# Kernel optimization log

Hardware: AMD Instinct MI355X
Metric: run time of the kernel (lower is better)

## Reference

```python
import jax, jax.numpy as jnp
import numpy as np

IN_DIM, H_DIM, EMB_DIM, CHEB_K = 2, 64, 10, 3
B, L, N = 16, 12, 2048
CAT = IN_DIM + H_DIM


def setup_inputs() -> dict:
    key = jax.random.key(0)
    ks = jax.random.split(key, 7)
    x = jax.random.normal(ks[0], (B, L, N, IN_DIM), dtype=jnp.float32)
    node_embs = jax.random.normal(ks[1], (N, EMB_DIM), dtype=jnp.float32)
    As = jax.random.uniform(ks[2], (N, N), dtype=jnp.float32) / N  # row-stochastic-ish support
    # NAPL parameter pools (AGCRN-style): per-gate weight/bias pools indexed by node embedding
    s = 0.1
    Wg_pool = jax.random.normal(ks[3], (EMB_DIM, CHEB_K, CAT, 2 * H_DIM), dtype=jnp.float32) * s
    bg_pool = jax.random.normal(ks[4], (EMB_DIM, 2 * H_DIM), dtype=jnp.float32) * s
    Wc_pool = jax.random.normal(ks[5], (EMB_DIM, CHEB_K, CAT, H_DIM), dtype=jnp.float32) * s
    bc_pool = jax.random.normal(ks[6], (EMB_DIM, H_DIM), dtype=jnp.float32) * s
    return {"x": x, "node_embs": node_embs, "As": As,
            "Wg_pool": Wg_pool, "bg_pool": bg_pool,
            "Wc_pool": Wc_pool, "bc_pool": bc_pool}


def _cheb_supports(A, k):
    # T0 = I, T1 = A, T_j = 2 A T_{j-1} - T_{j-2}
    n = A.shape[0]
    Ts = [jnp.eye(n, dtype=A.dtype), A]
    for _ in range(2, k):
        Ts.append(2.0 * A @ Ts[-1] - Ts[-2])
    return jnp.stack(Ts[:k], axis=0)  # (K, N, N)


def _napl_conv(xin, supports, Wn, bn):
    # xin: (B,N,Ci); supports: (K,N,N); Wn: (N,K,Ci,Co); bn: (N,Co)
    xg = jnp.einsum('knm,bmc->bnkc', supports, xin)
    return jnp.einsum('bnki,nkio->bno', xg, Wn) + bn


def reference(x, node_embs, As, Wg_pool, bg_pool, Wc_pool, bc_pool):
    supports = _cheb_supports(As, CHEB_K)
    # node-adaptive parameters (time-invariant: hoist out of the recurrence)
    Wg = jnp.einsum('nd,dkio->nkio', node_embs, Wg_pool)  # (N,K,CAT,2H)
    bg = node_embs @ bg_pool                               # (N,2H)
    Wc = jnp.einsum('nd,dkio->nkio', node_embs, Wc_pool)  # (N,K,CAT,H)
    bc = node_embs @ bc_pool                               # (N,H)

    def step(h_prev, x_t):
        cat = jnp.concatenate([h_prev, x_t], axis=-1)      # (B,N,CAT)
        gate = jax.nn.sigmoid(_napl_conv(cat, supports, Wg, bg))
        r_t, u_t = jnp.split(gate, 2, axis=-1)
        cat2 = jnp.concatenate([r_t * h_prev, x_t], axis=-1)
        c_t = jnp.tanh(_napl_conv(cat2, supports, Wc, bc))
        h_t = u_t * h_prev + (1.0 - u_t) * c_t
        return h_t, h_t

    h0 = jnp.zeros((x.shape[0], x.shape[2], H_DIM), dtype=x.dtype)
    x_time = jnp.moveaxis(x, 1, 0)                          # (L,B,N,C)
    h_n, outs = jax.lax.scan(step, h0, x_time)
    output = jnp.moveaxis(outs, 0, 1)                       # (B,L,N,H)
    return output, h_n
```

## Files before the change

### kernel.cpp

```cpp
#include <hip/hip_runtime.h>
#include <cstdint>
#include <cstddef>

typedef _Float16 h16;
typedef h16 v8h __attribute__((ext_vector_type(8)));
typedef h16 v4h __attribute__((ext_vector_type(4)));
typedef float v4f __attribute__((ext_vector_type(4)));

constexpr int NN = 2048;
constexpr float INV_N = 1.0f / 2048.0f;
constexpr int LP = 72;

#define MFMA16(a, b, c) __builtin_amdgcn_mfma_f32_16x16x32_f16((a), (b), (c), 0, 0, 0)

__global__ void fill_k(float* __restrict__ o, float v, size_t ntot) {
  size_t i = (size_t)blockIdx.x * 256 + threadIdx.x;
  if (i < ntot) o[i] = v;
}


__global__ void prep_Asplit_k(const float* __restrict__ A,
                              h16* __restrict__ hi, h16* __restrict__ lo) {
  int tid = blockIdx.x * 256 + threadIdx.x;
  float v = A[tid] * 2048.0f;
  h16 h = (h16)v;
  hi[tid] = h;
  lo[tid] = (h16)(v - (float)h);
}

__global__ void prep_AsTsplit_k(const float* __restrict__ A,
                                h16* __restrict__ hi, h16* __restrict__ lo) {
  int tid = blockIdx.x * 256 + threadIdx.x;
  int t = tid & 2047, j = tid >> 11;
  float v = A[(size_t)t * NN + j] * 2048.0f;
  h16 h = (h16)v;
  hi[(size_t)j * NN + t] = h;
  lo[(size_t)j * NN + t] = (h16)(v - (float)h);
}

__global__ void prep_x0split_k(const float* __restrict__ x,
                               h16* __restrict__ hi, h16* __restrict__ lo) {
  int tid = blockIdx.x * 256 + threadIdx.x;
  int n = tid & 2047, c = tid >> 11;
  int ii = c & 1, b = (c >> 1) & 15, lt = c >> 5;
  float v = x[(((size_t)(b * 12 + lt)) * NN + n) * 2 + ii];
  h16 h = (h16)v;
  hi[tid] = h;
  lo[tid] = (h16)(v - (float)h);
}

template<int CO>
__global__ void prep_wpack_k(const float* __restrict__ Wp,
                             h16* __restrict__ Ph, h16* __restrict__ Pl) {
  int tid = blockIdx.x * 256 + threadIdx.x;
  int c = tid & 7;
  int ln = (tid >> 3) & 63;
  int rest = tid >> 9;
  int b = rest & 3;
  int kk = (rest >> 2) & 1;
  int r3 = rest >> 3;
  int t = r3 % 30;
  int g = r3 / 30;
  int o = g * 64 + b * 16 + (ln & 15);
  int kcol = (t / 3) * 192 + (t % 3) * 64 + kk * 32 + (ln >> 4) * 8 + c;
  int d = kcol / 192, rem = kcol - d * 192;
  int jb = rem >> 6, i = rem & 63;
  float v;
  if (jb == 0)
    v = Wp[((size_t)((d * 3 + 0) * 66 + i)) * CO + o] -
        Wp[((size_t)((d * 3 + 2) * 66 + i)) * CO + o];
  else if (jb == 1)
    v = Wp[((size_t)((d * 3 + 1) * 66 + i)) * CO + o];
  else
    v = 2.f * Wp[((size_t)((d * 3 + 2) * 66 + i)) * CO + o];
  h16 h = (h16)v;
  Ph[tid] = h;
  Pl[tid] = (h16)(v - (float)h);
}

template<int CO>
__global__ void prep_wx_k(const float* __restrict__ E, const float* __restrict__ Wp,
                          float* __restrict__ Wx) {
  int tid = blockIdx.x * 256 + threadIdx.x;
  int o = tid & (CO - 1), t6 = (tid / CO) % 6, n = tid / (6 * CO);
  int k = t6 >> 1, ii = t6 & 1;
  float s = 0.f;
  for (int d = 0; d < 10; ++d) {
    float p0 = Wp[((size_t)((d * 3 + 0) * 66 + 64 + ii)) * CO + o];
    float p1 = Wp[((size_t)((d * 3 + 1) * 66 + 64 + ii)) * CO + o];
    float p2 = Wp[((size_t)((d * 3 + 2) * 66 + 64 + ii)) * CO + o];
    float v = (k == 0) ? (p0 - p2) : (k == 1 ? p1 : 2.f * p2);
    s += E[n * 10 + d] * v;
  }
  Wx[tid] = s;
}

template<int CO>
__global__ void prep_b_k(const float* __restrict__ E, const float* __restrict__ bp,
                         float* __restrict__ bv) {
  int tid = blockIdx.x * 256 + threadIdx.x;
  int o = tid & (CO - 1), n = tid / CO;
  float s = 0.f;
  for (int d = 0; d < 10; ++d) s += E[n * 10 + d] * bp[d * CO + o];
  bv[tid] = s;
}

template<int OM>
__global__ __launch_bounds__(256, 4) void sgemm_k(
    const h16* __restrict__ Ih, const h16* __restrict__ Il,
    const h16* __restrict__ Bh, const h16* __restrict__ Bl,
    float* __restrict__ oF, h16* __restrict__ oH, h16* __restrict__ oL,
    float* __restrict__ xsv, int xoff) {
  const int m0 = blockIdx.x * 64, n0 = blockIdx.y * 64;
  __shared__ __align__(16) h16 sAh[64 * LP], sAl[64 * LP];
  __shared__ __align__(16) h16 sBh[64 * LP], sBl[64 * LP];
  const int tid = threadIdx.x, lane = tid & 63, w = tid >> 6;
  const int wm = w >> 1, wn = w & 1;
  v4f acc[2][2] = {};
  const int sr = tid >> 2, sc = (tid & 3) * 16;
  v8h rah0 = *(const v8h*)(Ih + (size_t)(m0 + sr) * NN + sc);
  v8h rah1 = *(const v8h*)(Ih + (size_t)(m0 + sr) * NN + sc + 8);
  v8h ral0 = *(const v8h*)(Il + (size_t)(m0 + sr) * NN + sc);
  v8h ral1 = *(const v8h*)(Il + (size_t)(m0 + sr) * NN + sc + 8);
  v8h rbh0 = *(const v8h*)(Bh + (size_t)(n0 + sr) * NN + sc);
  v8h rbh1 = *(const v8h*)(Bh + (size_t)(n0 + sr) * NN + sc + 8);
  v8h rbl0 = *(const v8h*)(Bl + (size_t)(n0 + sr) * NN + sc);
  v8h rbl1 = *(const v8h*)(Bl + (size_t)(n0 + sr) * NN + sc + 8);
  for (int kt = 0; kt < NN; kt += 64) {
    __syncthreads();
    *(v8h*)(sAh + sr * LP + sc) = rah0;
    *(v8h*)(sAh + sr * LP + sc + 8) = rah1;
    *(v8h*)(sAl + sr * LP + sc) = ral0;
    *(v8h*)(sAl + sr * LP + sc + 8) = ral1;
    *(v8h*)(sBh + sr * LP + sc) = rbh0;
    *(v8h*)(sBh + sr * LP + sc + 8) = rbh1;
    *(v8h*)(sBl + sr * LP + sc) = rbl0;
    *(v8h*)(sBl + sr * LP + sc + 8) = rbl1;
    __syncthreads();
    if (kt + 64 < NN) {
      const int k2 = kt + 64 + sc;
      rah0 = *(const v8h*)(Ih + (size_t)(m0 + sr) * NN + k2);
      rah1 = *(const v8h*)(Ih + (size_t)(m0 + sr) * NN + k2 + 8);
      ral0 = *(const v8h*)(Il + (size_t)(m0 + sr) * NN + k2);
      ral1 = *(const v8h*)(Il + (size_t)(m0 + sr) * NN + k2 + 8);
      rbh0 = *(const v8h*)(Bh + (size_t)(n0 + sr) * NN + k2);
      rbh1 = *(const v8h*)(Bh + (size_t)(n0 + sr) * NN + k2 + 8);
      rbl0 = *(const v8h*)(Bl + (size_t)(n0 + sr) * NN + k2);
      rbl1 = *(const v8h*)(Bl + (size_t)(n0 + sr) * NN + k2 + 8);
    }
#pragma unroll
    for (int kk = 0; kk < 2; ++kk) {
      const int ko = kk * 32 + (lane >> 4) * 8;
      const int rs = lane & 15;
      v8h Ah0 = *(const v8h*)(sAh + (wm * 32 + rs) * LP + ko);
      v8h Ah1 = *(const v8h*)(sAh + (wm * 32 + 16 + rs) * LP + ko);
      v8h Al0 = *(const v8h*)(sAl + (wm * 32 + rs) * LP + ko);
      v8h Al1 = *(const v8h*)(sAl + (wm * 32 + 16 + rs) * LP + ko);
      v8h Bh0 = *(const v8h*)(sBh + (wn * 32 + rs) * LP + ko);
      v8h Bh1 = *(const v8h*)(sBh + (wn * 32 + 16 + rs) * LP + ko);
      v8h Bl0 = *(const v8h*)(sBl + (wn * 32 + rs) * LP + ko);
      v8h Bl1 = *(const v8h*)(sBl + (wn * 32 + 16 + rs) * LP + ko);
      acc[0][0] = MFMA16(Ah0, Bh0, acc[0][0]);
      acc[0][1] = MFMA16(Ah0, Bh1, acc[0][1]);
      acc[1][0] = MFMA16(Ah1, Bh0, acc[1][0]);
      acc[1][1] = MFMA16(Ah1, Bh1, acc[1][1]);
      acc[0][0] = MFMA16(Al0, Bh0, acc[0][0]);
      acc[0][1] = MFMA16(Al0, Bh1, acc[0][1]);
      acc[1][0] = MFMA16(Al1, Bh0, acc[1][0]);
      acc[1][1] = MFMA16(Al1, Bh1, acc[1][1]);
      acc[0][0] = MFMA16(Ah0, Bl0, acc[0][0]);
      acc[0][1] = MFMA16(Ah0, Bl1, acc[0][1]);
      acc[1][0] = MFMA16(Ah1, Bl0, acc[1][0]);
      acc[1][1] = MFMA16(Ah1, Bl1, acc[1][1]);
    }
  }
  const int l15 = lane & 15, l4 = (lane >> 4) * 4;
#pragma unroll
  for (int ni = 0; ni < 2; ++ni) {
    const int n = n0 + wn * 32 + ni * 16 + l15;
#pragma unroll
    for (int mi = 0; mi < 2; ++mi) {
      const int cb = m0 + wm * 32 + mi * 16 + l4;
      float vv[4];
#pragma unroll
      for (int r = 0; r < 4; ++r) {
        vv[r] = acc[mi][ni][r] * INV_N;
        if constexpr (OM & 1) oF[(size_t)(cb + r) * NN + n] = vv[r];
        if constexpr (OM & 2) {
          h16 h = (h16)vv[r];
          oH[(size_t)(cb + r) * NN + n] = h;
          oL[(size_t)(cb + r) * NN + n] = (h16)(vv[r] - (float)h);
        }
      }
      if constexpr (OM & 4) {
        const int n2 = n & 2047;
        const int xo = xoff + ((n >> 11) << 6);
        v4f pv = {vv[0], vv[1], vv[2], vv[3]};
        *(v4f*)(xsv + ((size_t)(cb >> 6) * 2048 + n2) * 192 + xo + (cb & 63)) = pv;
      }
    }
  }
}

__global__ __launch_bounds__(64) void mgate_k(
    const float* __restrict__ xs, const h16* __restrict__ Bph, const h16* __restrict__ Bpl,
    const float* __restrict__ E, const float* __restrict__ bgv,
    const float* __restrict__ Wx, const float* __restrict__ x,
    const float* __restrict__ X1t, const float* __restrict__ X2t,
    float* __restrict__ RHs, float* __restrict__ ubuf,
    h16* __restrict__ HRh, h16* __restrict__ HRl, int lt) {
  const int R0 = blockIdx.x * 32;
  const int gy = blockIdx.y, ob = gy * 64;
  const int bl = R0 >> 11, n0 = R0 & 2047;
  const int lane = threadIdx.x;
  const int rs = lane & 15, q = lane >> 4;
  float e0[10], e1[10];
#pragma unroll
  for (int d = 0; d < 10; ++d) {
    e0[d] = E[(size_t)(n0 + rs) * 10 + d];
    e1[d] = E[(size_t)(n0 + 16 + rs) * 10 + d];
  }
  const float* a0base = xs + (size_t)(R0 + rs) * 192;
  const float* a1base = xs + (size_t)(R0 + 16 + rs) * 192;
  const h16* pbh = Bph + (size_t)gy * 122880 + lane * 8;
  const h16* pbl = Bpl + (size_t)gy * 122880 + lane * 8;
  v4f acc[2][4] = {};
  int d = 0, jb = 0;
  for (int t = 0; t < 30; ++t) {
    const float ed0 = e0[d], ed1 = e1[d];
#pragma unroll
    for (int kk = 0; kk < 2; ++kk) {
      const int co = jb * 64 + kk * 32 + q * 8;
      v4f x00 = *(const v4f*)(a0base + co);
      v4f x01 = *(const v4f*)(a0base + co + 4);
      v4f x10 = *(const v4f*)(a1base + co);
      v4f x11 = *(const v4f*)(a1base + co + 4);
      v8h Ah0, Al0, Ah1, Al1;
#pragma unroll
      for (int i = 0; i < 4; ++i) {
        float v = x00[i] * ed0; h16 hh = (h16)v; Ah0[i] = hh; Al0[i] = (h16)(v - (float)hh);
        v = x01[i] * ed0; hh = (h16)v; Ah0[4 + i] = hh; Al0[4 + i] = (h16)(v - (float)hh);
        v = x10[i] * ed1; hh = (h16)v; Ah1[i] = hh; Al1[i] = (h16)(v - (float)hh);
        v = x11[i] * ed1; hh = (h16)v; Ah1[4 + i] = hh; Al1[4 + i] = (h16)(v - (float)hh);
      }
      const size_t boff = (size_t)((t * 2 + kk) * 4) * 512;
#pragma unroll
      for (int b = 0; b < 4; ++b) {
        v8h Bh = *(const v8h*)(pbh + boff + b * 512);
        v8h Bl = *(const v8h*)(pbl + boff + b * 512);
        acc[0][b] = MFMA16(Ah0, Bh, acc[0][b]);
        acc[1][b] = MFMA16(Ah1, Bh, acc[1][b]);
        acc[0][b] = MFMA16(Al0, Bh, acc[0][b]);
        acc[1][b] = MFMA16(Al1, Bh, acc[1][b]);
        acc[0][b] = MFMA16(Ah0, Bl, acc[0][b]);
        acc[1][b] = MFMA16(Ah1, Bl, acc[1][b]);
        acc[0][b] = MFMA16(Al0, Bl, acc[0][b]);
        acc[1][b] = MFMA16(Al1, Bl, acc[1][b]);
      }
    }
    if (++jb == 3) { jb = 0; ++d; }
  }
  const size_t xbase = ((size_t)(bl * 12 + lt)) * NN;
  const size_t c1 = ((size_t)(lt * 16 + bl)) * 2;
#pragma unroll
  for (int mi = 0; mi < 2; ++mi) {
#pragma unroll
    for (int b = 0; b < 4; ++b) {
      const int o = ob + b * 16 + rs;
      float rhv[4];
#pragma unroll
      for (int r = 0; r < 4; ++r) {
        const int Rl = mi * 16 + q * 4 + r;
        const int n = n0 + Rl;
        const size_t R = (size_t)R0 + Rl;
        const float x0a = x[(xbase + n) * 2 + 0];
        const float x0b = x[(xbase + n) * 2 + 1];
        const float x1a = X1t[c1 * NN + n];
        const float x1b = X1t[(c1 + 1) * NN + n];
        const float x2a = X2t[c1 * NN + n];
        const float x2b = X2t[(c1 + 1) * NN + n];
        const float* wx = Wx + (size_t)n * 768;
        float pre = acc[mi][b][r] + bgv[(size_t)n * 128 + o]
                  + x0a * wx[o]       + x0b * wx[128 + o]
                  + x1a * wx[256 + o] + x1b * wx[384 + o]
                  + x2a * wx[512 + o] + x2b * wx[640 + o];
        const float g = 1.f / (1.f + expf(-pre));
        if (gy == 0) {
          const float rh = g * xs[R * 192 + o];
          RHs[(size_t)bl * 1572864 + (size_t)n * 64 + o] = rh;
          rhv[r] = rh;
        } else {
          ubuf[R * 64 + (o - 64)] = g;
        }
      }
      if (gy == 0) {
        const int nb = n0 + mi * 16 + q * 4;
        v4h ph, pl;
#pragma unroll
        for (int r = 0; r < 4; ++r) {
          h16 hh = (h16)rhv[r];
          ph[r] = hh;
          pl[r] = (h16)(rhv[r] - (float)hh);
        }
        *(v4h*)(HRh + (size_t)(bl * 64 + o) * 2048 + nb) = ph;
        *(v4h*)(HRl + (size_t)(bl * 64 + o) * 2048 + nb) = pl;
      }
    }
  }
}

__global__ __launch_bounds__(64) void mcand_k(
    float* __restrict__ xs, const float* __restrict__ RHs,
    const h16* __restrict__ Bph, const h16* __restrict__ Bpl,
    const float* __restrict__ E, const float* __restrict__ bcv,
    const float* __restrict__ Wx, const float* __restrict__ x,
    const float* __restrict__ X1t, const float* __restrict__ X2t,
    const float* __restrict__ ubuf, h16* __restrict__ HRh, h16* __restrict__ HRl,
    float* __restrict__ out, int lt) {
  const int R0 = blockIdx.x * 32;
  const int bl = R0 >> 11, n0 = R0 & 2047;
  const int lane = threadIdx.x;
  const int rs = lane & 15, q = lane >> 4;
  float e0[10], e1[10];
#pragma unroll
  for (int d = 0; d < 10; ++d) {
    e0[d] = E[(size_t)(n0 + rs) * 10 + d];
    e1[d] = E[(size_t)(n0 + 16 + rs) * 10 + d];
  }
  const float* rh0 = RHs + (size_t)bl * 1572864 + (size_t)(n0 + rs) * 64;
  const float* rh1 = RHs + (size_t)bl * 1572864 + (size_t)(n0 + 16 + rs) * 64;
  const float* xs0 = xs + (size_t)(R0 + rs) * 192;
  const float* xs1 = xs + (size_t)(R0 + 16 + rs) * 192;
  const h16* pbh = Bph + lane * 8;
  const h16* pbl = Bpl + lane * 8;
  v4f acc[2][4] = {};
  int d = 0, jb = 0;
  for (int t = 0; t < 30; ++t) {
    const float ed0 = e0[d], ed1 = e1[d];
#pragma unroll
    for (int kk = 0; kk < 2; ++kk) {
      const int cq = kk * 32 + q * 8;
      const float* s0 = (jb == 0) ? (rh0 + cq) : (xs0 + jb * 64 + cq);
      const float* s1 = (jb == 0) ? (rh1 + cq) : (xs1 + jb * 64 + cq);
      v4f x00 = *(const v4f*)s0;
      v4f x01 = *(const v4f*)(s0 + 4);
      v4f x10 = *(const v4f*)s1;
      v4f x11 = *(const v4f*)(s1 + 4);
      v8h Ah0, Al0, Ah1, Al1;
#pragma unroll
      for (int i = 0; i < 4; ++i) {
        float v = x00[i] * ed0; h16 hh = (h16)v; Ah0[i] = hh; Al0[i] = (h16)(v - (float)hh);
        v = x01[i] * ed0; hh = (h16)v; Ah0[4 + i] = hh; Al0[4 + i] = (h16)(v - (float)hh);
        v = x10[i] * ed1; hh = (h16)v; Ah1[i] = hh; Al1[i] = (h16)(v - (float)hh);
        v = x11[i] * ed1; hh = (h16)v; Ah1[4 + i] = hh; Al1[4 + i] = (h16)(v - (float)hh);
      }
      const size_t boff = (size_t)((t * 2 + kk) * 4) * 512;
#pragma unroll
      for (int b = 0; b < 4; ++b) {
        v8h Bh = *(const v8h*)(pbh + boff + b * 512);
        v8h Bl = *(const v8h*)(pbl + boff + b * 512);
        acc[0][b] = MFMA16(Ah0, Bh, acc[0][b]);
        acc[1][b] = MFMA16(Ah1, Bh, acc[1][b]);
        acc[0][b] = MFMA16(Al0, Bh, acc[0][b]);
        acc[1][b] = MFMA16(Al1, Bh, acc[1][b]);
        acc[0][b] = MFMA16(Ah0, Bl, acc[0][b]);
        acc[1][b] = MFMA16(Ah1, Bl, acc[1][b]);
        acc[0][b] = MFMA16(Al0, Bl, acc[0][b]);
        acc[1][b] = MFMA16(Al1, Bl, acc[1][b]);
      }
    }
    if (++jb == 3) { jb = 0; ++d; }
  }
  const size_t xbase = ((size_t)(bl * 12 + lt)) * NN;
  const size_t c1 = ((size_t)(lt * 16 + bl)) * 2;
#pragma unroll
  for (int mi = 0; mi < 2; ++mi) {
#pragma unroll
    for (int b = 0; b < 4; ++b) {
      const int o = b * 16 + rs;
      float hnv[4];
#pragma unroll
      for (int r = 0; r < 4; ++r) {
        const int Rl = mi * 16 + q * 4 + r;
        const int n = n0 + Rl;
        const size_t R = (size_t)R0 + Rl;
        const float x0a = x[(xbase + n) * 2 + 0];
        const float x0b = x[(xbase + n) * 2 + 1];
        const float x1a = X1t[c1 * NN + n];
        const float x1b = X1t[(c1 + 1) * NN + n];
        const float x2a = X2t[c1 * NN + n];
        const float x2b = X2t[(c1 + 1) * NN + n];
        const float* wx = Wx + (size_t)n * 384;
        float pre = acc[mi][b][r] + bcv[(size_t)n * 64 + o]
                  + x0a * wx[o]       + x0b * wx[64 + o]
                  + x1a * wx[128 + o] + x1b * wx[192 + o]
                  + x2a * wx[256 + o] + x2b * wx[320 + o];
        const float cv = tanhf(pre);
        const float u = ubuf[R * 64 + o];
        const float hold = xs[R * 192 + o];
        const float hn = u * hold + (1.f - u) * cv;
        hnv[r] = hn;
        xs[R * 192 + o] = hn;
        out[(xbase + n) * 64 + o] = hn;
      }
      const int nb = n0 + mi * 16 + q * 4;
      v4h ph, pl;
#pragma unroll
      for (int r = 0; r < 4; ++r) {
        h16 hh = (h16)hnv[r];
        ph[r] = hh;
        pl[r] = (h16)(hnv[r] - (float)hh);
      }
      *(v4h*)(HRh + (size_t)(bl * 64 + o) * 2048 + nb) = ph;
      *(v4h*)(HRl + (size_t)(bl * 64 + o) * 2048 + nb) = pl;
    }
  }
}

__global__ void hn_gather_k(const float* __restrict__ xs, float* __restrict__ dst) {
  int i = blockIdx.x * 256 + threadIdx.x;
  dst[i] = xs[(size_t)(i >> 6) * 192 + (i & 63)];
}

extern "C" void kernel_launch(void* const* d_in, const int* in_sizes, int n_in,
                              void* d_out, int out_size, void* d_ws, size_t ws_size,
                              hipStream_t stream) {
  float* out = (float*)d_out;

  const bool in_ok = (n_in == 7) &&
      in_sizes[0] == 786432 && in_sizes[1] == 20480 && in_sizes[2] == 4194304 &&
      in_sizes[3] == 253440 && in_sizes[4] == 1280 &&
      in_sizes[5] == 126720 && in_sizes[6] == 640 && out_size == 27262976;
  if (!in_ok) {
    fill_k<<<(out_size + 255) / 256, 256, 0, stream>>>(out, 77.0f, (size_t)out_size);
    return;
  }
  constexpr size_t NEED = 85884928;
  if (ws_size < NEED) {
    fill_k<<<106496, 256, 0, stream>>>(out, 42.0f, 27262976);
    return;
  }

  const float* x   = (const float*)d_in[0];
  const float* E   = (const float*)d_in[1];
  const float* A   = (const float*)d_in[2];
  const float* Wgp = (const float*)d_in[3];
  const float* bgp = (const float*)d_in[4];
  const float* Wcp = (const float*)d_in[5];
  const float* bcp = (const float*)d_in[6];

  char* p = (char*)d_ws;
  auto carve = [&](size_t bytes) { char* r = p; p += bytes; return r; };
  h16*   ABh  = (h16*)carve(16777216);
  h16*   ABl  = (h16*)carve(16777216);
  float* X1t  = (float*)carve(3145728);
  float* X2t  = (float*)carve(3145728);
  h16*   WgTh = (h16*)carve(491520);
  h16*   WgTl = (h16*)carve(491520);
  h16*   WcTh = (h16*)carve(245760);
  h16*   WcTl = (h16*)carve(245760);
  float* WxG  = (float*)carve(6291456);
  float* WxC  = (float*)carve(3145728);
  float* bgv  = (float*)carve(1048576);
  float* bcv  = (float*)carve(524288);
  float* xs   = (float*)carve(25165824);
  h16*   HRh  = (h16*)carve(4194304);
  h16*   HRl  = (h16*)carve(4194304);
  float* RHs  = out + 1441792;
  float* ubuf = out + 25165824;
  h16* AsTh = (h16*)xs;
  h16* AsTl = (h16*)((char*)xs + 8388608);
  h16* X0h  = (h16*)((char*)xs + 16777216);
  h16* X0l  = (h16*)((char*)xs + 18350080);
  h16* X1h  = (h16*)((char*)xs + 19922944);
  h16* X1l  = (h16*)((char*)xs + 21495808);

  prep_Asplit_k<<<16384, 256, 0, stream>>>(A, ABh, ABl);
  prep_AsTsplit_k<<<16384, 256, 0, stream>>>(A, AsTh, AsTl);
  prep_wpack_k<128><<<960, 256, 0, stream>>>(Wgp, WgTh, WgTl);
  prep_wpack_k<64><<<480, 256, 0, stream>>>(Wcp, WcTh, WcTl);
  prep_wx_k<128><<<6144, 256, 0, stream>>>(E, Wgp, WxG);
  prep_wx_k<64><<<3072, 256, 0, stream>>>(E, Wcp, WxC);
  prep_b_k<128><<<1024, 256, 0, stream>>>(E, bgp, bgv);
  prep_b_k<64><<<512, 256, 0, stream>>>(E, bcp, bcv);
  sgemm_k<2><<<dim3(32, 32), 256, 0, stream>>>(ABh, ABl, AsTh, AsTl,
                                               nullptr, ABh + 4194304, ABl + 4194304,
                                               nullptr, 0);
  prep_x0split_k<<<3072, 256, 0, stream>>>(x, X0h, X0l);
  sgemm_k<3><<<dim3(6, 32), 256, 0, stream>>>(X0h, X0l, ABh, ABl, X1t, X1h, X1l, nullptr, 0);
  sgemm_k<1><<<dim3(6, 32), 256, 0, stream>>>(X1h, X1l, ABh, ABl, X2t, nullptr, nullptr, nullptr, 0);

  hipMemsetAsync(xs, 0, 25165824, stream);
  hipMemsetAsync(HRh, 0, 4194304, stream);
  hipMemsetAsync(HRl, 0, 4194304, stream);
  for (int lt = 0; lt < 12; ++lt) {
    sgemm_k<4><<<dim3(16, 64), 256, 0, stream>>>(HRh, HRl, ABh, ABl,
                                                 nullptr, nullptr, nullptr, xs, 64);
    mgate_k<<<dim3(1024, 2), 64, 0, stream>>>(xs, WgTh, WgTl, E, bgv, WxG, x, X1t, X2t,
                                              RHs, ubuf, HRh, HRl, lt);
    sgemm_k<4><<<dim3(16, 64), 256, 0, stream>>>(HRh, HRl, ABh, ABl,
                                                 nullptr, nullptr, nullptr, xs, 64);
    mcand_k<<<1024, 64, 0, stream>>>(xs, RHs, WcTh, WcTl, E, bcv, WxC, x, X1t, X2t,
                                     ubuf, HRh, HRl, out, lt);
  }
  hn_gather_k<<<8192, 256, 0, stream>>>(xs, out + 25165824);
}
```

Baseline: 4.187 ms.

## Stage scaled split-half A tiles in LDS shared by four waves in gate/candidate kernels

The gate and candidate MFMA kernels move from one-wave blocks to four-wave blocks. Each block converts its 32-row A tile once into hi/lo fp16 halves in double-buffered shared memory, and each wave computes a slice of output columns from it. The gate kernel no longer needs a second grid dimension, and the A conversion and global reads are no longer repeated per output-column group. The cost is a __syncthreads per K step, extra LDS traffic, and fewer blocks in flight for the candidate kernel.

After: 3.600 ms. 1.16x faster.

```diff
diff --git a/kernel.cpp b/kernel.cpp
--- a/kernel.cpp
+++ b/kernel.cpp
@@ -202,7 +202,7 @@
   }
 }
 
-__global__ __launch_bounds__(64) void mgate_k(
+__global__ __launch_bounds__(256) void mgate_k(
     const float* __restrict__ xs, const h16* __restrict__ Bph, const h16* __restrict__ Bpl,
     const float* __restrict__ E, const float* __restrict__ bgv,
     const float* __restrict__ Wx, const float* __restrict__ x,
@@ -210,52 +210,58 @@
     float* __restrict__ RHs, float* __restrict__ ubuf,
     h16* __restrict__ HRh, h16* __restrict__ HRl, int lt) {
   const int R0 = blockIdx.x * 32;
-  const int gy = blockIdx.y, ob = gy * 64;
   const int bl = R0 >> 11, n0 = R0 & 2047;
-  const int lane = threadIdx.x;
+  __shared__ __align__(16) h16 sAh[2 * 32 * LP], sAl[2 * 32 * LP];
+  const int tid = threadIdx.x, lane = tid & 63, w = tid >> 6;
   const int rs = lane & 15, q = lane >> 4;
-  float e0[10], e1[10];
-#pragma unroll
-  for (int d = 0; d < 10; ++d) {
-    e0[d] = E[(size_t)(n0 + rs) * 10 + d];
-    e1[d] = E[(size_t)(n0 + 16 + rs) * 10 + d];
-  }
-  const float* a0base = xs + (size_t)(R0 + rs) * 192;
-  const float* a1base = xs + (size_t)(R0 + 16 + rs) * 192;
-  const h16* pbh = Bph + (size_t)gy * 122880 + lane * 8;
-  const h16* pbl = Bpl + (size_t)gy * 122880 + lane * 8;
-  v4f acc[2][4] = {};
+  const int g = w >> 1, bsel = (w & 1) * 2, ob = w * 32;
+  const int asr = tid >> 3, asc = (tid & 7) * 8;
+  const float* arow = xs + (size_t)(R0 + asr) * 192 + asc;
+  const float* erow = E + (size_t)(n0 + asr) * 10;
+  const h16* pbh = Bph + (size_t)(g * 30) * 4096 + lane * 8;
+  const h16* pbl = Bpl + (size_t)(g * 30) * 4096 + lane * 8;
+  v4f acc[2][2] = {};
   int d = 0, jb = 0;
   for (int t = 0; t < 30; ++t) {
-    const float ed0 = e0[d], ed1 = e1[d];
+    v8h Bh[2][2], Bl[2][2];
+#pragma unroll
+    for (int kk = 0; kk < 2; ++kk)
+#pragma unroll
+      for (int bi = 0; bi < 2; ++bi) {
+        const size_t off = (size_t)t * 4096 + kk * 2048 + (bsel + bi) * 512;
+        Bh[kk][bi] = *(const v8h*)(pbh + off);
+        Bl[kk][bi] = *(const v8h*)(pbl + off);
+      }
+    const float e = erow[d];
+    v4f a0 = *(const v4f*)(arow + jb * 64);
+    v4f a1 = *(const v4f*)(arow + jb * 64 + 4);
+    v8h ah, al;
+#pragma unroll
+    for (int i = 0; i < 4; ++i) {
+      float v = a0[i] * e; h16 hh = (h16)v; ah[i] = hh; al[i] = (h16)(v - (float)hh);
+      v = a1[i] * e; hh = (h16)v; ah[4 + i] = hh; al[4 + i] = (h16)(v - (float)hh);
+    }
+    const int bo = (t & 1) * (32 * LP);
+    *(v8h*)(sAh + bo + asr * LP + asc) = ah;
+    *(v8h*)(sAl + bo + asr * LP + asc) = al;
+    __syncthreads();
 #pragma unroll
     for (int kk = 0; kk < 2; ++kk) {
-      const int co = jb * 64 + kk * 32 + q * 8;
-      v4f x00 = *(const v4f*)(a0base + co);
-      v4f x01 = *(const v4f*)(a0base + co + 4);
-      v4f x10 = *(const v4f*)(a1base + co);
-      v4f x11 = *(const v4f*)(a1base + co + 4);
-      v8h Ah0, Al0, Ah1, Al1;
-#pragma unroll
-      for (int i = 0; i < 4; ++i) {
-        float v = x00[i] * ed0; h16 hh = (h16)v; Ah0[i] = hh; Al0[i] = (h16)(v - (float)hh);
-        v = x01[i] * ed0; hh = (h16)v; Ah0[4 + i] = hh; Al0[4 + i] = (h16)(v - (float)hh);
-        v = x10[i] * ed1; hh = (h16)v; Ah1[i] = hh; Al1[i] = (h16)(v - (float)hh);
-        v = x11[i] * ed1; hh = (h16)v; Ah1[4 + i] = hh; Al1[4 + i] = (h16)(v - (float)hh);
-      }
-      const size_t boff = (size_t)((t * 2 + kk) * 4) * 512;
-#pragma unroll
-      for (int b = 0; b < 4; ++b) {
-        v8h Bh = *(const v8h*)(pbh + boff + b * 512);
-        v8h Bl = *(const v8h*)(pbl + boff + b * 512);
-        acc[0][b] = MFMA16(Ah0, Bh, acc[0][b]);
-        acc[1][b] = MFMA16(Ah1, Bh, acc[1][b]);
-        acc[0][b] = MFMA16(Al0, Bh, acc[0][b]);
-        acc[1][b] = MFMA16(Al1, Bh, acc[1][b]);
-        acc[0][b] = MFMA16(Ah0, Bl, acc[0][b]);
-        acc[1][b] = MFMA16(Ah1, Bl, acc[1][b]);
-        acc[0][b] = MFMA16(Al0, Bl, acc[0][b]);
-        acc[1][b] = MFMA16(Al1, Bl, acc[1][b]);
+      const int ko = kk * 32 + q * 8;
+      v8h Ah0 = *(const v8h*)(sAh + bo + rs * LP + ko);
+      v8h Ah1 = *(const v8h*)(sAh + bo + (16 + rs) * LP + ko);
+      v8h Al0 = *(const v8h*)(sAl + bo + rs * LP + ko);
+      v8h Al1 = *(const v8h*)(sAl + bo + (16 + rs) * LP + ko);
+#pragma unroll
+      for (int bi = 0; bi < 2; ++bi) {
+        acc[0][bi] = MFMA16(Ah0, Bh[kk][bi], acc[0][bi]);
+        acc[1][bi] = MFMA16(Ah1, Bh[kk][bi], acc[1][bi]);
+        acc[0][bi] = MFMA16(Al0, Bh[kk][bi], acc[0][bi]);
+        acc[1][bi] = MFMA16(Al1, Bh[kk][bi], acc[1][bi]);
+        acc[0][bi] = MFMA16(Ah0, Bl[kk][bi], acc[0][bi]);
+        acc[1][bi] = MFMA16(Ah1, Bl[kk][bi], acc[1][bi]);
+        acc[0][bi] = MFMA16(Al0, Bl[kk][bi], acc[0][bi]);
+        acc[1][bi] = MFMA16(Al1, Bl[kk][bi], acc[1][bi]);
       }
     }
     if (++jb == 3) { jb = 0; ++d; }
@@ -265,8 +271,8 @@
 #pragma unroll
   for (int mi = 0; mi < 2; ++mi) {
 #pragma unroll
-    for (int b = 0; b < 4; ++b) {
-      const int o = ob + b * 16 + rs;
+    for (int bi = 0; bi < 2; ++bi) {
+      const int o = ob + bi * 16 + rs;
       float rhv[4];
 #pragma unroll
       for (int r = 0; r < 4; ++r) {
@@ -280,20 +286,20 @@
         const float x2a = X2t[c1 * NN + n];
         const float x2b = X2t[(c1 + 1) * NN + n];
         const float* wx = Wx + (size_t)n * 768;
-        float pre = acc[mi][b][r] + bgv[(size_t)n * 128 + o]
+        float pre = acc[mi][bi][r] + bgv[(size_t)n * 128 + o]
                   + x0a * wx[o]       + x0b * wx[128 + o]
                   + x1a * wx[256 + o] + x1b * wx[384 + o]
                   + x2a * wx[512 + o] + x2b * wx[640 + o];
-        const float g = 1.f / (1.f + expf(-pre));
-        if (gy == 0) {
-          const float rh = g * xs[R * 192 + o];
+        const float gg = 1.f / (1.f + expf(-pre));
+        if (o < 64) {
+          const float rh = gg * xs[R * 192 + o];
           RHs[(size_t)bl * 1572864 + (size_t)n * 64 + o] = rh;
           rhv[r] = rh;
         } else {
-          ubuf[R * 64 + (o - 64)] = g;
+          ubuf[R * 64 + (o - 64)] = gg;
         }
       }
-      if (gy == 0) {
+      if (o < 64) {
         const int nb = n0 + mi * 16 + q * 4;
         v4h ph, pl;
 #pragma unroll
@@ -309,7 +315,7 @@
   }
 }
 
-__global__ __launch_bounds__(64) void mcand_k(
+__global__ __launch_bounds__(256) void mcand_k(
     float* __restrict__ xs, const float* __restrict__ RHs,
     const h16* __restrict__ Bph, const h16* __restrict__ Bpl,
     const float* __restrict__ E, const float* __restrict__ bcv,
@@ -319,101 +325,97 @@
     float* __restrict__ out, int lt) {
   const int R0 = blockIdx.x * 32;
   const int bl = R0 >> 11, n0 = R0 & 2047;
-  const int lane = threadIdx.x;
+  __shared__ __align__(16) h16 sAh[2 * 32 * LP], sAl[2 * 32 * LP];
+  const int tid = threadIdx.x, lane = tid & 63, w = tid >> 6;
   const int rs = lane & 15, q = lane >> 4;
-  float e0[10], e1[10];
-#pragma unroll
-  for (int d = 0; d < 10; ++d) {
-    e0[d] = E[(size_t)(n0 + rs) * 10 + d];
-    e1[d] = E[(size_t)(n0 + 16 + rs) * 10 + d];
-  }
-  const float* rh0 = RHs + (size_t)bl * 1572864 + (size_t)(n0 + rs) * 64;
-  const float* rh1 = RHs + (size_t)bl * 1572864 + (size_t)(n0 + 16 + rs) * 64;
-  const float* xs0 = xs + (size_t)(R0 + rs) * 192;
-  const float* xs1 = xs + (size_t)(R0 + 16 + rs) * 192;
+  const int asr = tid >> 3, asc = (tid & 7) * 8;
+  const float* erow = E + (size_t)(n0 + asr) * 10;
+  const float* rhrow = RHs + (size_t)bl * 1572864 + (size_t)(n0 + asr) * 64 + asc;
+  const float* xsrow = xs + (size_t)(R0 + asr) * 192 + asc;
   const h16* pbh = Bph + lane * 8;
   const h16* pbl = Bpl + lane * 8;
-  v4f acc[2][4] = {};
+  v4f acc[2] = {};
   int d = 0, jb = 0;
   for (int t = 0; t < 30; ++t) {
-    const float ed0 = e0[d], ed1 = e1[d];
+    v8h Bh[2], Bl[2];
 #pragma unroll
     for (int kk = 0; kk < 2; ++kk) {
-      const int cq = kk * 32 + q * 8;
-      const float* s0 = (jb == 0) ? (rh0 + cq) : (xs0 + jb * 64 + cq);
-      const float* s1 = (jb == 0) ? (rh1 + cq) : (xs1 + jb * 64 + cq);
-      v4f x00 = *(const v4f*)s0;
-      v4f x01 = *(const v4f*)(s0 + 4);
-      v4f x10 = *(const v4f*)s1;
-      v4f x11 = *(const v4f*)(s1 + 4);
-      v8h Ah0, Al0, Ah1, Al1;
-#pragma unroll
-      for (int i = 0; i < 4; ++i) {
-        float v = x00[i] * ed0; h16 hh = (h16)v; Ah0[i] = hh; Al0[i] = (h16)(v - (float)hh);
-        v = x01[i] * ed0; hh = (h16)v; Ah0[4 + i] = hh; Al0[4 + i] = (h16)(v - (float)hh);
-        v = x10[i] * ed1; hh = (h16)v; Ah1[i] = hh; Al1[i] = (h16)(v - (float)hh);
-        v = x11[i] * ed1; hh = (h16)v; Ah1[4 + i] = hh; Al1[4 + i] = (h16)(v - (float)hh);
-      }
-      const size_t boff = (size_t)((t * 2 + kk) * 4) * 512;
-#pragma unroll
-      for (int b = 0; b < 4; ++b) {
-        v8h Bh = *(const v8h*)(pbh + boff + b * 512);
-        v8h Bl = *(const v8h*)(pbl + boff + b * 512);
-        acc[0][b] = MFMA16(Ah0, Bh, acc[0][b]);
-        acc[1][b] = MFMA16(Ah1, Bh, acc[1][b]);
-        acc[0][b] = MFMA16(Al0, Bh, acc[0][b]);
-        acc[1][b] = MFMA16(Al1, Bh, acc[1][b]);
-        acc[0][b] = MFMA16(Ah0, Bl, acc[0][b]);
-        acc[1][b] = MFMA16(Ah1, Bl, acc[1][b]);
-        acc[0][b] = MFMA16(Al0, Bl, acc[0][b]);
-        acc[1][b] = MFMA16(Al1, Bl, acc[1][b]);
-      }
+      const size_t off = (size_t)t * 4096 + kk * 2048 + w * 512;
+      Bh[kk] = *(const v8h*)(pbh + off);
+      Bl[kk] = *(const v8h*)(pbl + off);
+    }
+    const float e = erow[d];
+    const float* src = (jb == 0) ? rhrow : (xsrow + jb * 64);
+    v4f a0 = *(const v4f*)src;
+    v4f a1 = *(const v4f*)(src + 4);
+    v8h ah, al;
+#pragma unroll
+    for (int i = 0; i < 4; ++i) {
+      float v = a0[i] * e; h16 hh = (h16)v; ah[i] = hh; al[i] = (h16)(v - (float)hh);
+      v = a1[i] * e; hh = (h16)v; ah[4 + i] = hh; al[4 + i] = (h16)(v - (float)hh);
+    }
+    const int bo = (t & 1) * (32 * LP);
+    *(v8h*)(sAh + bo + asr * LP + asc) = ah;
+    *(v8h*)(sAl + bo + asr * LP + asc) = al;
+    __syncthreads();
+#pragma unroll
+    for (int kk = 0; kk < 2; ++kk) {
+      const int ko = kk * 32 + q * 8;
+      v8h Ah0 = *(const v8h*)(sAh + bo + rs * LP + ko);
+      v8h Ah1 = *(const v8h*)(sAh + bo + (16 + rs) * LP + ko);
+      v8h Al0 = *(const v8h*)(sAl + bo + rs * LP + ko);
+      v8h Al1 = *(const v8h*)(sAl + bo + (16 + rs) * LP + ko);
+      acc[0] = MFMA16(Ah0, Bh[kk], acc[0]);
+      acc[1] = MFMA16(Ah1, Bh[kk], acc[1]);
+      acc[0] = MFMA16(Al0, Bh[kk], acc[0]);
+      acc[1] = MFMA16(Al1, Bh[kk], acc[1]);
+      acc[0] = MFMA16(Ah0, Bl[kk], acc[0]);
+      acc[1] = MFMA16(Ah1, Bl[kk], acc[1]);
+      acc[0] = MFMA16(Al0, Bl[kk], acc[0]);
+      acc[1] = MFMA16(Al1, Bl[kk], acc[1]);
     }
     if (++jb == 3) { jb = 0; ++d; }
   }
   const size_t xbase = ((size_t)(bl * 12 + lt)) * NN;
   const size_t c1 = ((size_t)(lt * 16 + bl)) * 2;
+  const int o = w * 16 + rs;
 #pragma unroll
   for (int mi = 0; mi < 2; ++mi) {
-#pragma unroll
-    for (int b = 0; b < 4; ++b) {
-      const int o = b * 16 + rs;
-      float hnv[4];
-#pragma unroll
-      for (int r = 0; r < 4; ++r) {
-        const int Rl = mi * 16 + q * 4 + r;
-        const int n = n0 + Rl;
-        const size_t R = (size_t)R0 + Rl;
-        const float x0a = x[(xbase + n) * 2 + 0];
-        const float x0b = x[(xbase + n) * 2 + 1];
-        const float x1a = X1t[c1 * NN + n];
-        const float x1b = X1t[(c1 + 1) * NN + n];
-        const float x2a = X2t[c1 * NN + n];
-        const float x2b = X2t[(c1 + 1) * NN + n];
-        const float* wx = Wx + (size_t)n * 384;
-        float pre = acc[mi][b][r] + bcv[(size_t)n * 64 + o]
-                  + x0a * wx[o]       + x0b * wx[64 + o]
-                  + x1a * wx[128 + o] + x1b * wx[192 + o]
-                  + x2a * wx[256 + o] + x2b * wx[320 + o];
-        const float cv = tanhf(pre);
-        const float u = ubuf[R * 64 + o];
-        const float hold = xs[R * 192 + o];
-        const float hn = u * hold + (1.f - u) * cv;
-        hnv[r] = hn;
-        xs[R * 192 + o] = hn;
-        out[(xbase + n) * 64 + o] = hn;
-      }
-      const int nb = n0 + mi * 16 + q * 4;
-      v4h ph, pl;
-#pragma unroll
-      for (int r = 0; r < 4; ++r) {
-        h16 hh = (h16)hnv[r];
-        ph[r] = hh;
-        pl[r] = (h16)(hnv[r] - (float)hh);
-      }
-      *(v4h*)(HRh + (size_t)(bl * 64 + o) * 2048 + nb) = ph;
-      *(v4h*)(HRl + (size_t)(bl * 64 + o) * 2048 + nb) = pl;
-    }
+    float hnv[4];
+#pragma unroll
+    for (int r = 0; r < 4; ++r) {
+      const int Rl = mi * 16 + q * 4 + r;
+      const int n = n0 + Rl;
+      const size_t R = (size_t)R0 + Rl;
+      const float x0a = x[(xbase + n) * 2 + 0];
+      const float x0b = x[(xbase + n) * 2 + 1];
+      const float x1a = X1t[c1 * NN + n];
+      const float x1b = X1t[(c1 + 1) * NN + n];
+      const float x2a = X2t[c1 * NN + n];
+      const float x2b = X2t[(c1 + 1) * NN + n];
+      const float* wx = Wx + (size_t)n * 384;
+      float pre = acc[mi][r] + bcv[(size_t)n * 64 + o]
+                + x0a * wx[o]       + x0b * wx[64 + o]
+                + x1a * wx[128 + o] + x1b * wx[192 + o]
+                + x2a * wx[256 + o] + x2b * wx[320 + o];
+      const float cv = tanhf(pre);
+      const float u = ubuf[R * 64 + o];
+      const float hold = xs[R * 192 + o];
+      const float hn = u * hold + (1.f - u) * cv;
+      hnv[r] = hn;
+      xs[R * 192 + o] = hn;
+      out[(xbase + n) * 64 + o] = hn;
+    }
+    const int nb = n0 + mi * 16 + q * 4;
+    v4h ph, pl;
+#pragma unroll
+    for (int r = 0; r < 4; ++r) {
+      h16 hh = (h16)hnv[r];
+      ph[r] = hh;
+      pl[r] = (h16)(hnv[r] - (float)hh);
+    }
+    *(v4h*)(HRh + (size_t)(bl * 64 + o) * 2048 + nb) = ph;
+    *(v4h*)(HRl + (size_t)(bl * 64 + o) * 2048 + nb) = pl;
   }
 }
 
@@ -496,12 +498,12 @@
   for (int lt = 0; lt < 12; ++lt) {
     sgemm_k<4><<<dim3(16, 64), 256, 0, stream>>>(HRh, HRl, ABh, ABl,
                                                  nullptr, nullptr, nullptr, xs, 64);
-    mgate_k<<<dim3(1024, 2), 64, 0, stream>>>(xs, WgTh, WgTl, E, bgv, WxG, x, X1t, X2t,
-                                              RHs, ubuf, HRh, HRl, lt);
+    mgate_k<<<1024, 256, 0, stream>>>(xs, WgTh, WgTl, E, bgv, WxG, x, X1t, X2t,
+                                      RHs, ubuf, HRh, HRl, lt);
     sgemm_k<4><<<dim3(16, 64), 256, 0, stream>>>(HRh, HRl, ABh, ABl,
                                                  nullptr, nullptr, nullptr, xs, 64);
-    mcand_k<<<1024, 64, 0, stream>>>(xs, RHs, WcTh, WcTl, E, bcv, WxC, x, X1t, X2t,
-                                     ubuf, HRh, HRl, out, lt);
+    mcand_k<<<1024, 256, 0, stream>>>(xs, RHs, WcTh, WcTl, E, bcv, WxC, x, X1t, X2t,
+                                      ubuf, HRh, HRl, out, lt);
   }
   hn_gather_k<<<8192, 256, 0, stream>>>(xs, out + 25165824);
 }
```
